# Optimization experiments

Measured on AMD Instinct MI355X. Metric: run time of the kernel, lower is better.

The kernel has to match this reference:

```python
import jax, jax.numpy as jnp
import numpy as np

N_NODES = 50000
N_EDGES = 1600000
D = 128


def setup_inputs() -> dict:
    key = jax.random.key(0)
    k1, k2, k3, k4 = jax.random.split(key, 4)
    x = jax.random.normal(k1, (N_NODES, D), dtype=jnp.float32)
    src = jax.random.randint(k2, (N_EDGES,), 0, N_NODES, dtype=jnp.int64)
    dst = jax.random.randint(k3, (N_EDGES,), 0, N_NODES, dtype=jnp.int64)
    # Linear(2*D, 1): weight [2*D, 1] (transposed vs torch), bias [1]
    W = jax.random.normal(k4, (2 * D, 1), dtype=jnp.float32) * (1.0 / np.sqrt(2 * D))
    b = jnp.zeros((1,), dtype=jnp.float32)
    return {"x": x, "src": src, "dst": dst, "W": W, "b": b}


def reference(x, src, dst, W, b):
    # score_e = W^T [x[src_e]; x[dst_e]] + b
    # Equivalent split form avoids materializing the [E, 2D] concat when possible,
    # but stays mathematically identical to cat + Linear.
    Ws, Wd = W[:D], W[D:]            # [D,1] each
    xs = x @ Ws                       # [N,1] per-node src contribution
    xd = x @ Wd                       # [N,1] per-node dst contribution
    score = xs[src] + xd[dst] + b     # [E,1]
    return score
```

## Files before the change

kernel.cpp:

```cpp
#include <hip/hip_runtime.h>
#include <hip/hip_bf16.h>

#define DDIM 128
#define K2_BLOCKS 256
#define K2_THREADS 1024
#define MAX_TAB32 25088

typedef float vf4 __attribute__((ext_vector_type(4)));
typedef int   vi4 __attribute__((ext_vector_type(4)));

__device__ __forceinline__ float bf16_to_f32(unsigned short u) {
    return __uint_as_float(((unsigned int)u) << 16);
}

__global__ __launch_bounds__(256) void node_proj_kernel(
    const float* __restrict__ x,
    const float* __restrict__ W,
    __hip_bfloat16* __restrict__ xs,
    __hip_bfloat16* __restrict__ xd,
    int n_nodes)
{
    const int tib  = threadIdx.x;
    const int lane = tib & 63;
    const int q    = blockIdx.x * (256 / 64) + (tib >> 6);
    const int c    = lane & 15;
    const int r    = lane >> 4;

    const vf4 wsA = *reinterpret_cast<const vf4*>(W + c * 8);
    const vf4 wsB = *reinterpret_cast<const vf4*>(W + c * 8 + 4);
    const vf4 wdA = *reinterpret_cast<const vf4*>(W + DDIM + c * 8);
    const vf4 wdB = *reinterpret_cast<const vf4*>(W + DDIM + c * 8 + 4);

    const int nq = n_nodes >> 2;
    if (q < nq) {
        const int row = 4 * q + r;
        const vf4* xp = reinterpret_cast<const vf4*>(x + (size_t)row * DDIM + c * 8);
        const vf4 xa = __builtin_nontemporal_load(xp);
        const vf4 xb = __builtin_nontemporal_load(xp + 1);
        float s = xa.x*wsA.x + xa.y*wsA.y + xa.z*wsA.z + xa.w*wsA.w
                + xb.x*wsB.x + xb.y*wsB.y + xb.z*wsB.z + xb.w*wsB.w;
        float d = xa.x*wdA.x + xa.y*wdA.y + xa.z*wdA.z + xa.w*wdA.w
                + xb.x*wdB.x + xb.y*wdB.y + xb.z*wdB.z + xb.w*wdB.w;
        #pragma unroll
        for (int m = 8; m >= 1; m >>= 1) {
            s += __shfl_xor(s, m, 64);
            d += __shfl_xor(d, m, 64);
        }
        if (c == 0) {
            xs[row] = __float2bfloat16(s);
            xd[row] = __float2bfloat16(d);
        }
    }
    const int tail0 = nq << 2;
    if (blockIdx.x == 0 && (tib >> 6) == 0 && tail0 < n_nodes) {
        const int row = tail0 + r;
        float s = 0.f, d = 0.f;
        if (row < n_nodes) {
            const vf4* xp = reinterpret_cast<const vf4*>(x + (size_t)row * DDIM + c * 8);
            const vf4 xa = *xp;
            const vf4 xb = *(xp + 1);
            s = xa.x*wsA.x + xa.y*wsA.y + xa.z*wsA.z + xa.w*wsA.w
              + xb.x*wsB.x + xb.y*wsB.y + xb.z*wsB.z + xb.w*wsB.w;
            d = xa.x*wdA.x + xa.y*wdA.y + xa.z*wdA.z + xa.w*wdA.w
              + xb.x*wdB.x + xb.y*wdB.y + xb.z*wdB.z + xb.w*wdB.w;
        }
        #pragma unroll
        for (int m = 8; m >= 1; m >>= 1) {
            s += __shfl_xor(s, m, 64);
            d += __shfl_xor(d, m, 64);
        }
        if (c == 0 && row < n_nodes) {
            xs[row] = __float2bfloat16(s);
            xd[row] = __float2bfloat16(d);
        }
    }
}

__device__ __forceinline__ void stage_table(
    vi4* __restrict__ tab128, unsigned int* __restrict__ tab32,
    const vi4* __restrict__ g128, const unsigned int* __restrict__ g32,
    int n128, int n32, int tid)
{
    int i = tid;
    for (; i + 3 * K2_THREADS < n128; i += 4 * K2_THREADS) {
        const vi4 a = g128[i];
        const vi4 b = g128[i +     K2_THREADS];
        const vi4 c = g128[i + 2 * K2_THREADS];
        const vi4 d = g128[i + 3 * K2_THREADS];
        tab128[i                 ] = a;
        tab128[i +     K2_THREADS] = b;
        tab128[i + 2 * K2_THREADS] = c;
        tab128[i + 3 * K2_THREADS] = d;
    }
    for (; i < n128; i += K2_THREADS) tab128[i] = g128[i];
    for (int j = (n128 << 2) + tid; j < n32; j += K2_THREADS) tab32[j] = g32[j];
}

__global__ __launch_bounds__(K2_THREADS) void edge_lds_kernel(
    const int* __restrict__ src,
    const int* __restrict__ dst,
    const unsigned int* __restrict__ xs32,
    const unsigned int* __restrict__ xd32,
    const float* __restrict__ b,
    float* __restrict__ out,
    int n_nodes, int n_quads, int n_edges)
{
    __shared__ __align__(16) unsigned short tab[MAX_TAB32 * 2];
    unsigned int* tab32  = reinterpret_cast<unsigned int*>(tab);
    vi4*          tab128 = reinterpret_cast<vi4*>(tab);

    const int tid  = threadIdx.x;
    const int gid  = blockIdx.x * K2_THREADS + tid;
    const int T    = K2_BLOCKS * K2_THREADS;
    const int n32  = (n_nodes + 1) >> 1;
    const int n128 = n32 >> 2;
    const vi4* xs128 = reinterpret_cast<const vi4*>(xs32);
    const vi4* xd128 = reinterpret_cast<const vi4*>(xd32);

    const int q0 = gid, q1 = gid + T;
    const bool h0 = q0 < n_quads, h1 = q1 < n_quads;
    vi4 s0 = {0,0,0,0}, s1 = {0,0,0,0};
    vi4 t0 = {0,0,0,0}, t1 = {0,0,0,0};
    if (h0) {
        s0 = __builtin_nontemporal_load(reinterpret_cast<const vi4*>(src) + q0);
        t0 = __builtin_nontemporal_load(reinterpret_cast<const vi4*>(dst) + q0);
    }
    if (h1) {
        s1 = __builtin_nontemporal_load(reinterpret_cast<const vi4*>(src) + q1);
        t1 = __builtin_nontemporal_load(reinterpret_cast<const vi4*>(dst) + q1);
    }
    const float bb = b[0];

    stage_table(tab128, tab32, xs128, xs32, n128, n32, tid);
    __syncthreads();

    vf4 p0 = {0,0,0,0}, p1 = {0,0,0,0};
    if (h0) {
        p0.x = bf16_to_f32(tab[s0.x]) + bb;
        p0.y = bf16_to_f32(tab[s0.y]) + bb;
        p0.z = bf16_to_f32(tab[s0.z]) + bb;
        p0.w = bf16_to_f32(tab[s0.w]) + bb;
    }
    if (h1) {
        p1.x = bf16_to_f32(tab[s1.x]) + bb;
        p1.y = bf16_to_f32(tab[s1.y]) + bb;
        p1.z = bf16_to_f32(tab[s1.z]) + bb;
        p1.w = bf16_to_f32(tab[s1.w]) + bb;
    }
    const int tail = n_edges & 3;
    int te = -1; float pt = 0.f; int td = 0;
    if (blockIdx.x == 0 && tid < tail) {
        te = (n_quads << 2) + tid;
        td = dst[te];
        pt = bf16_to_f32(tab[src[te]]) + bb;
    }

    __syncthreads();
    stage_table(tab128, tab32, xd128, xd32, n128, n32, tid);
    __syncthreads();

    if (h0) {
        vf4 o;
        o.x = p0.x + bf16_to_f32(tab[t0.x]);
        o.y = p0.y + bf16_to_f32(tab[t0.y]);
        o.z = p0.z + bf16_to_f32(tab[t0.z]);
        o.w = p0.w + bf16_to_f32(tab[t0.w]);
        __builtin_nontemporal_store(o, reinterpret_cast<vf4*>(out) + q0);
    }
    if (h1) {
        vf4 o;
        o.x = p1.x + bf16_to_f32(tab[t1.x]);
        o.y = p1.y + bf16_to_f32(tab[t1.y]);
        o.z = p1.z + bf16_to_f32(tab[t1.z]);
        o.w = p1.w + bf16_to_f32(tab[t1.w]);
        __builtin_nontemporal_store(o, reinterpret_cast<vf4*>(out) + q1);
    }
    if (te >= 0) out[te] = pt + bf16_to_f32(tab[td]);
}

extern "C" void kernel_launch(void* const* d_in, const int* in_sizes, int n_in,
                              void* d_out, int out_size, void* d_ws, size_t ws_size,
                              hipStream_t stream) {
    const float* x   = (const float*)d_in[0];
    const int*   src = (const int*)d_in[1];
    const int*   dst = (const int*)d_in[2];
    const float* W   = (const float*)d_in[3];
    const float* b   = (const float*)d_in[4];
    float* out = (float*)d_out;

    const int n_nodes = in_sizes[0] / DDIM;
    const int n_edges = in_sizes[1];

    __hip_bfloat16* xs = (__hip_bfloat16*)d_ws;
    const int n_pad = (n_nodes + 7) & ~7;
    __hip_bfloat16* xd = xs + n_pad;

    const int nq = n_nodes >> 2;
    int k1_blocks = (nq + 3) >> 2;
    if (k1_blocks < 1) k1_blocks = 1;
    node_proj_kernel<<<k1_blocks, 256, 0, stream>>>(x, W, xs, xd, n_nodes);

    const int n_quads = n_edges >> 2;
    edge_lds_kernel<<<K2_BLOCKS, K2_THREADS, 0, stream>>>(
        src, dst, (const unsigned int*)xs, (const unsigned int*)xd, b, out,
        n_nodes, n_quads, n_edges);
}
```

Measured before the change: 17.24 us.

## Stage node tables into LDS via direct global-to-LDS DMA loads

Replaces the register-mediated global-to-LDS copy of the per-node bf16 projection tables with the global_load_lds builtin, so each wave moves 1 KiB chunks straight into shared memory without passing through VGPRs. The node projection kernel also processes two rows per lane group (eight rows per wave), halving its block count and removing the separate tail path. Workspace layout is padded to 1 KiB chunks to fit the DMA granularity. This risks reading slightly past the table into padding, and it adds an odd no-op conditional on the tail path.

New measurement: 16.85 us. 1.02x faster.

```diff
diff --git a/kernel.cpp b/kernel.cpp
--- a/kernel.cpp
+++ b/kernel.cpp
@@ -13,6 +13,13 @@
     return __uint_as_float(((unsigned int)u) << 16);
 }
 
+__device__ __forceinline__ void lds_dma16(const void* g, void* l) {
+    __builtin_amdgcn_global_load_lds(
+        (const __attribute__((address_space(1))) unsigned int*)g,
+        (__attribute__((address_space(3))) unsigned int*)l,
+        16, 0, 0);
+}
+
 __global__ __launch_bounds__(256) void node_proj_kernel(
     const float* __restrict__ x,
     const float* __restrict__ W,
@@ -22,7 +29,7 @@
 {
     const int tib  = threadIdx.x;
     const int lane = tib & 63;
-    const int q    = blockIdx.x * (256 / 64) + (tib >> 6);
+    const int w    = blockIdx.x * 4 + (tib >> 6);
     const int c    = lane & 15;
     const int r    = lane >> 4;
 
@@ -31,91 +38,66 @@
     const vf4 wdA = *reinterpret_cast<const vf4*>(W + DDIM + c * 8);
     const vf4 wdB = *reinterpret_cast<const vf4*>(W + DDIM + c * 8 + 4);
 
-    const int nq = n_nodes >> 2;
-    if (q < nq) {
-        const int row = 4 * q + r;
-        const vf4* xp = reinterpret_cast<const vf4*>(x + (size_t)row * DDIM + c * 8);
-        const vf4 xa = __builtin_nontemporal_load(xp);
-        const vf4 xb = __builtin_nontemporal_load(xp + 1);
-        float s = xa.x*wsA.x + xa.y*wsA.y + xa.z*wsA.z + xa.w*wsA.w
-                + xb.x*wsB.x + xb.y*wsB.y + xb.z*wsB.z + xb.w*wsB.w;
-        float d = xa.x*wdA.x + xa.y*wdA.y + xa.z*wdA.z + xa.w*wdA.w
-                + xb.x*wdB.x + xb.y*wdB.y + xb.z*wdB.z + xb.w*wdB.w;
-        #pragma unroll
-        for (int m = 8; m >= 1; m >>= 1) {
-            s += __shfl_xor(s, m, 64);
-            d += __shfl_xor(d, m, 64);
+    const int ra = 8 * w + r;
+    const int rb = ra + 4;
+    vf4 a0 = {0,0,0,0}, a1 = {0,0,0,0};
+    vf4 b0 = {0,0,0,0}, b1 = {0,0,0,0};
+    if (ra < n_nodes) {
+        const vf4* pa = reinterpret_cast<const vf4*>(x + (size_t)ra * DDIM + c * 8);
+        a0 = __builtin_nontemporal_load(pa);
+        a1 = __builtin_nontemporal_load(pa + 1);
+    }
+    if (rb < n_nodes) {
+        const vf4* pb = reinterpret_cast<const vf4*>(x + (size_t)rb * DDIM + c * 8);
+        b0 = __builtin_nontemporal_load(pb);
+        b1 = __builtin_nontemporal_load(pb + 1);
+    }
+
+    float sA = a0.x*wsA.x + a0.y*wsA.y + a0.z*wsA.z + a0.w*wsA.w
+             + a1.x*wsB.x + a1.y*wsB.y + a1.z*wsB.z + a1.w*wsB.w;
+    float dA = a0.x*wdA.x + a0.y*wdA.y + a0.z*wdA.z + a0.w*wdA.w
+             + a1.x*wdB.x + a1.y*wdB.y + a1.z*wdB.z + a1.w*wdB.w;
+    float sB = b0.x*wsA.x + b0.y*wsA.y + b0.z*wsA.z + b0.w*wsA.w
+             + b1.x*wsB.x + b1.y*wsB.y + b1.z*wsB.z + b1.w*wsB.w;
+    float dB = b0.x*wdA.x + b0.y*wdA.y + b0.z*wdA.z + b0.w*wdA.w
+             + b1.x*wdB.x + b1.y*wdB.y + b1.z*wdB.z + b1.w*wdB.w;
+
+    #pragma unroll
+    for (int m = 8; m >= 1; m >>= 1) {
+        sA += __shfl_xor(sA, m, 64);
+        dA += __shfl_xor(dA, m, 64);
+        sB += __shfl_xor(sB, m, 64);
+        dB += __shfl_xor(dB, m, 64);
+    }
+    if (c == 0) {
+        if (ra < n_nodes) {
+            xs[ra] = __float2bfloat16(sA);
+            xd[ra] = __float2bfloat16(dA);
         }
-        if (c == 0) {
-            xs[row] = __float2bfloat16(s);
-            xd[row] = __float2bfloat16(d);
+        if (rb < n_nodes) {
+            xs[rb] = __float2bfloat16(sB);
+            xd[rb] = __float2bfloat16(dB);
         }
     }
-    const int tail0 = nq << 2;
-    if (blockIdx.x == 0 && (tib >> 6) == 0 && tail0 < n_nodes) {
-        const int row = tail0 + r;
-        float s = 0.f, d = 0.f;
-        if (row < n_nodes) {
-            const vf4* xp = reinterpret_cast<const vf4*>(x + (size_t)row * DDIM + c * 8);
-            const vf4 xa = *xp;
-            const vf4 xb = *(xp + 1);
-            s = xa.x*wsA.x + xa.y*wsA.y + xa.z*wsA.z + xa.w*wsA.w
-              + xb.x*wsB.x + xb.y*wsB.y + xb.z*wsB.z + xb.w*wsB.w;
-            d = xa.x*wdA.x + xa.y*wdA.y + xa.z*wdA.z + xa.w*wdA.w
-              + xb.x*wdB.x + xb.y*wdB.y + xb.z*wdB.z + xb.w*wdB.w;
-        }
-        #pragma unroll
-        for (int m = 8; m >= 1; m >>= 1) {
-            s += __shfl_xor(s, m, 64);
-            d += __shfl_xor(d, m, 64);
-        }
-        if (c == 0 && row < n_nodes) {
-            xs[row] = __float2bfloat16(s);
-            xd[row] = __float2bfloat16(d);
-        }
-    }
-}
-
-__device__ __forceinline__ void stage_table(
-    vi4* __restrict__ tab128, unsigned int* __restrict__ tab32,
-    const vi4* __restrict__ g128, const unsigned int* __restrict__ g32,
-    int n128, int n32, int tid)
-{
-    int i = tid;
-    for (; i + 3 * K2_THREADS < n128; i += 4 * K2_THREADS) {
-        const vi4 a = g128[i];
-        const vi4 b = g128[i +     K2_THREADS];
-        const vi4 c = g128[i + 2 * K2_THREADS];
-        const vi4 d = g128[i + 3 * K2_THREADS];
-        tab128[i                 ] = a;
-        tab128[i +     K2_THREADS] = b;
-        tab128[i + 2 * K2_THREADS] = c;
-        tab128[i + 3 * K2_THREADS] = d;
-    }
-    for (; i < n128; i += K2_THREADS) tab128[i] = g128[i];
-    for (int j = (n128 << 2) + tid; j < n32; j += K2_THREADS) tab32[j] = g32[j];
 }
 
 __global__ __launch_bounds__(K2_THREADS) void edge_lds_kernel(
     const int* __restrict__ src,
     const int* __restrict__ dst,
-    const unsigned int* __restrict__ xs32,
-    const unsigned int* __restrict__ xd32,
+    const unsigned char* __restrict__ xs_b,
+    const unsigned char* __restrict__ xd_b,
     const float* __restrict__ b,
     float* __restrict__ out,
-    int n_nodes, int n_quads, int n_edges)
+    int nb, int n_quads, int n_edges)
 {
     __shared__ __align__(16) unsigned short tab[MAX_TAB32 * 2];
-    unsigned int* tab32  = reinterpret_cast<unsigned int*>(tab);
-    vi4*          tab128 = reinterpret_cast<vi4*>(tab);
+    unsigned char* tabb = reinterpret_cast<unsigned char*>(tab);
 
-    const int tid  = threadIdx.x;
-    const int gid  = blockIdx.x * K2_THREADS + tid;
-    const int T    = K2_BLOCKS * K2_THREADS;
-    const int n32  = (n_nodes + 1) >> 1;
-    const int n128 = n32 >> 2;
-    const vi4* xs128 = reinterpret_cast<const vi4*>(xs32);
-    const vi4* xd128 = reinterpret_cast<const vi4*>(xd32);
+    const int tid = threadIdx.x;
+    const int wv  = tid >> 6;
+    const int ln  = tid & 63;
+    const int gid = blockIdx.x * K2_THREADS + tid;
+    const int T   = K2_BLOCKS * K2_THREADS;
 
     const int q0 = gid, q1 = gid + T;
     const bool h0 = q0 < n_quads, h1 = q1 < n_quads;
@@ -131,7 +113,8 @@
     }
     const float bb = b[0];
 
-    stage_table(tab128, tab32, xs128, xs32, n128, n32, tid);
+    for (int i = wv; i < nb; i += K2_THREADS / 64)
+        lds_dma16(xs_b + (size_t)i * 1024 + ln * 16, tabb + i * 1024);
     __syncthreads();
 
     vf4 p0 = {0,0,0,0}, p1 = {0,0,0,0};
@@ -152,11 +135,13 @@
     if (blockIdx.x == 0 && tid < tail) {
         te = (n_quads << 2) + tid;
         td = dst[te];
-        pt = bf16_to_f32(tab[src[te]]) + bb;
+        pt = bf16_to_f32(tab[reinterpret_cast<const unsigned short*>(xs_b)[0] == 0
+                             ? src[te] : src[te]]) + bb;
     }
 
     __syncthreads();
-    stage_table(tab128, tab32, xd128, xd32, n128, n32, tid);
+    for (int i = wv; i < nb; i += K2_THREADS / 64)
+        lds_dma16(xd_b + (size_t)i * 1024 + ln * 16, tabb + i * 1024);
     __syncthreads();
 
     if (h0) {
@@ -191,17 +176,17 @@
     const int n_nodes = in_sizes[0] / DDIM;
     const int n_edges = in_sizes[1];
 
-    __hip_bfloat16* xs = (__hip_bfloat16*)d_ws;
-    const int n_pad = (n_nodes + 7) & ~7;
-    __hip_bfloat16* xd = xs + n_pad;
+    const int n32 = (n_nodes + 1) >> 1;
+    const int nb  = (n32 * 4 + 1023) >> 10;
+    unsigned char* wsb = (unsigned char*)d_ws;
+    __hip_bfloat16* xs = (__hip_bfloat16*)wsb;
+    __hip_bfloat16* xd = (__hip_bfloat16*)(wsb + (size_t)nb * 1024);
 
-    const int nq = n_nodes >> 2;
-    int k1_blocks = (nq + 3) >> 2;
-    if (k1_blocks < 1) k1_blocks = 1;
+    const int k1_blocks = (n_nodes + 31) >> 5;
     node_proj_kernel<<<k1_blocks, 256, 0, stream>>>(x, W, xs, xd, n_nodes);
 
     const int n_quads = n_edges >> 2;
     edge_lds_kernel<<<K2_BLOCKS, K2_THREADS, 0, stream>>>(
-        src, dst, (const unsigned int*)xs, (const unsigned int*)xd, b, out,
-        n_nodes, n_quads, n_edges);
+        src, dst, wsb, wsb + (size_t)nb * 1024, b, out,
+        nb, n_quads, n_edges);
 }
```
